# Kernel tuning notes

Measured on AMD Instinct MI355X. Metric: run time of the kernel, lower is better.

The kernel has to match this reference:

```python
import jax, jax.numpy as jnp
import numpy as np

B, S, D_MODEL = 2, 2048, 512
KEY_DIM, VALUE_DIM, OUTPUT_DIM, NUM_HEADS = 256, 256, 512, 8


def setup_inputs() -> dict:
    key = jax.random.key(0)
    ks = jax.random.split(key, 12)
    s = 0.02
    return {
        "V": jax.random.normal(ks[0], (B, S, D_MODEL), jnp.float32),
        "Q": jax.random.normal(ks[1], (B, S, D_MODEL), jnp.float32),
        "K": jax.random.normal(ks[2], (B, S, D_MODEL), jnp.float32),
        "mask": jax.random.normal(ks[3], (B, 1, S, S), jnp.float32),
        "Wq": jax.random.normal(ks[4], (D_MODEL, KEY_DIM), jnp.float32) * s,
        "bq": jnp.zeros((KEY_DIM,), jnp.float32),
        "Wk": jax.random.normal(ks[5], (D_MODEL, KEY_DIM), jnp.float32) * s,
        "bk": jnp.zeros((KEY_DIM,), jnp.float32),
        "Wv": jax.random.normal(ks[6], (D_MODEL, VALUE_DIM), jnp.float32) * s,
        "bv": jnp.zeros((VALUE_DIM,), jnp.float32),
        "Wo": jax.random.normal(ks[7], (VALUE_DIM, OUTPUT_DIM), jnp.float32) * s,
        "bo": jnp.zeros((OUTPUT_DIM,), jnp.float32),
    }


def _split_heads(x, num_heads):
    # [B, S, H*d] -> [B, H, S, d]
    b, s, hd = x.shape
    return x.reshape(b, s, num_heads, hd // num_heads).transpose(0, 2, 1, 3)


def reference(V, Q, K, mask, Wq, bq, Wk, bk, Wv, bv, Wo, bo):
    denom = jnp.sqrt(jnp.float32(KEY_DIM))  # NOTE: full key_dim, as in source
    q = _split_heads(Q @ Wq + bq, NUM_HEADS)  # [B,H,S,dk]
    k = _split_heads(K @ Wk + bk, NUM_HEADS)
    scores = jnp.einsum("bhqd,bhkd->bhqk", q, k) / denom
    scores = scores + mask  # soft (additive) mask
    weights = jax.nn.softmax(scores, axis=-1)
    v = _split_heads(V @ Wv + bv, NUM_HEADS)  # [B,H,S,dv]
    ctx = jnp.einsum("bhqk,bhkd->bhqd", weights, v)  # [B,H,S,dv]
    b, h, s, d = ctx.shape
    ctx = ctx.transpose(0, 2, 1, 3).reshape(b, s, h * d)  # merge heads
    return ctx @ Wo + bo
```

## Files before the change

### kernel.cpp

```cpp
#include <hip/hip_runtime.h>

typedef __attribute__((ext_vector_type(8))) short bf16x8;
typedef __attribute__((ext_vector_type(4))) float f32x4;

#define B_  2
#define S_  2048
#define DM  512
#define KD  256
#define HD  32
#define NH  8

__device__ __forceinline__ float bf2f(ushort u) {
    return __uint_as_float(((uint)u) << 16);
}
__device__ __forceinline__ ushort f2bf(float f) {
    uint x = __float_as_uint(f);
    return (ushort)((x + 0x7fffu + ((x >> 16) & 1u)) >> 16);
}
#define MFMA __builtin_amdgcn_mfma_f32_16x16x32_bf16

__device__ __forceinline__ int detect_isbf(const ushort* __restrict__ q)
{
    int lane = threadIdx.x & 63;
    int e = (q[lane] >> 7) & 0xFF;
    unsigned long long m = __ballot(e >= 100 && e <= 133);
    return __popcll(m) >= 58;
}

__global__ __launch_bounds__(256) void transpose_w(
    const void* __restrict__ Wq, const void* __restrict__ Wk, const void* __restrict__ Wv,
    const void* __restrict__ Wo,
    const void* __restrict__ bq, const void* __restrict__ bk,
    const void* __restrict__ bv, const void* __restrict__ bo,
    const ushort* __restrict__ qsrc,
    ushort* __restrict__ Wt, ushort* __restrict__ Wot, float* __restrict__ biasf)
{
    int isbf = detect_isbf(qsrc);
    int bid = blockIdx.x;
    if (bid >= 512) {
        for (int i = threadIdx.x; i < 1280; i += 256) {
            const void* bp; int off;
            if (i < 256)      { bp = bq; off = i; }
            else if (i < 512) { bp = bk; off = i - 256; }
            else if (i < 768) { bp = bv; off = i - 512; }
            else              { bp = bo; off = i - 768; }
            biasf[i] = isbf ? bf2f(((const ushort*)bp)[off]) : ((const float*)bp)[off];
        }
        return;
    }
    const void* W; int R, C; ushort* T;
    int m = bid >> 7, tix = bid & 127;
    if (m < 3) { W = (m == 0) ? Wq : (m == 1) ? Wk : Wv; R = 512; C = 256; T = Wt + m * 131072; }
    else       { W = Wo; R = 256; C = 512; T = Wot; }
    int tilesPerRow = C >> 5;
    int r0 = (tix / tilesPerRow) * 32, c0 = (tix % tilesPerRow) * 32;
    __shared__ float lds[32][33];
    int t = threadIdx.x;
    int rr = t >> 3, cc = (t & 7) * 4;
    if (isbf) {
        const ushort* Ws = (const ushort*)W;
        #pragma unroll
        for (int j = 0; j < 4; ++j) lds[rr][cc + j] = bf2f(Ws[(size_t)(r0 + rr) * C + c0 + cc + j]);
    } else {
        float4 v = *(const float4*)((const float*)W + (size_t)(r0 + rr) * C + c0 + cc);
        lds[rr][cc + 0] = v.x; lds[rr][cc + 1] = v.y; lds[rr][cc + 2] = v.z; lds[rr][cc + 3] = v.w;
    }
    __syncthreads();
    ushort4 o;
    o.x = f2bf(lds[cc + 0][rr]); o.y = f2bf(lds[cc + 1][rr]);
    o.z = f2bf(lds[cc + 2][rr]); o.w = f2bf(lds[cc + 3][rr]);
    *(ushort4*)(T + (size_t)(c0 + rr) * R + r0 + cc) = o;
}

__global__ __launch_bounds__(256) void qkv_gemm(
    const void* __restrict__ Q, const void* __restrict__ K, const void* __restrict__ V,
    const ushort* __restrict__ Wt, const float* __restrict__ biasf,
    ushort* __restrict__ qh, ushort* __restrict__ kh, ushort* __restrict__ vT)
{
    int isbf = detect_isbf((const ushort*)Q);
    int y = blockIdx.y;
    const void* X = (y == 0) ? Q : (y == 1) ? K : V;
    int wave = threadIdx.x >> 6, lane = threadIdx.x & 63;
    int l16 = lane & 15, quad = lane >> 4;
    int m0 = blockIdx.x * 32;
    int n0 = wave * 64;
    const ushort* W = Wt + (size_t)y * (256 * 512);

    auto loadA = [&](int ks, bf16x8* a) {
        #pragma unroll
        for (int i = 0; i < 2; ++i) {
            if (isbf) {
                a[i] = *(const bf16x8*)((const ushort*)X + (size_t)(m0 + 16 * i + l16) * 512 + ks + quad * 8);
            } else {
                const float* p = (const float*)X + (size_t)(m0 + 16 * i + l16) * 512 + ks + quad * 8;
                float4 f0 = *(const float4*)p, f1 = *(const float4*)(p + 4);
                bf16x8 v8;
                v8[0] = (short)f2bf(f0.x); v8[1] = (short)f2bf(f0.y);
                v8[2] = (short)f2bf(f0.z); v8[3] = (short)f2bf(f0.w);
                v8[4] = (short)f2bf(f1.x); v8[5] = (short)f2bf(f1.y);
                v8[6] = (short)f2bf(f1.z); v8[7] = (short)f2bf(f1.w);
                a[i] = v8;
            }
        }
    };
    auto loadB = [&](int ks, bf16x8* b) {
        #pragma unroll
        for (int j = 0; j < 4; ++j)
            b[j] = *(const bf16x8*)(W + (size_t)(n0 + 16 * j + l16) * 512 + ks + quad * 8);
    };

    f32x4 acc[2][4] = {};
    bf16x8 aC[2], bC[4], aN[2], bN[4];
    loadA(0, aC); loadB(0, bC);
    for (int ks = 0; ks < 512; ks += 32) {
        if (ks + 32 < 512) { loadA(ks + 32, aN); loadB(ks + 32, bN); }
        #pragma unroll
        for (int i = 0; i < 2; ++i)
            #pragma unroll
            for (int j = 0; j < 4; ++j)
                acc[i][j] = MFMA(aC[i], bC[j], acc[i][j], 0, 0, 0);
        aC[0] = aN[0]; aC[1] = aN[1];
        #pragma unroll
        for (int j = 0; j < 4; ++j) bC[j] = bN[j];
    }
    if (y < 2) {
        ushort* out = (y == 0) ? qh : kh;
        #pragma unroll
        for (int i = 0; i < 2; ++i) {
            #pragma unroll
            for (int j = 0; j < 4; ++j) {
                int n = n0 + 16 * j + l16;
                float bs = biasf[y * 256 + n];
                int h = n >> 5, d = n & 31;
                #pragma unroll
                for (int r = 0; r < 4; ++r) {
                    int rg = m0 + 16 * i + quad * 4 + r;
                    int bb = rg >> 11, ss = rg & 2047;
                    out[((((size_t)bb * NH + h) * S_ + ss) << 5) + d] = f2bf(acc[i][j][r] + bs);
                }
            }
        }
    } else {
        #pragma unroll
        for (int i = 0; i < 2; ++i) {
            int rg0 = m0 + 16 * i + quad * 4;
            int bb = rg0 >> 11, s0 = rg0 & 2047;
            #pragma unroll
            for (int j = 0; j < 4; ++j) {
                int n = n0 + 16 * j + l16;
                float bs = biasf[2 * 256 + n];
                int h = n >> 5, d = n & 31;
                ushort4 o;
                o.x = f2bf(acc[i][j][0] + bs); o.y = f2bf(acc[i][j][1] + bs);
                o.z = f2bf(acc[i][j][2] + bs); o.w = f2bf(acc[i][j][3] + bs);
                *(ushort4*)(vT + (((size_t)(bb * NH + h) * HD + d) * S_) + s0) = o;
            }
        }
    }
}

__global__ __launch_bounds__(256) void attn(
    const ushort* __restrict__ qh, const ushort* __restrict__ kh,
    const ushort* __restrict__ vT, const void* __restrict__ maskp,
    float* __restrict__ pO, float* __restrict__ pl)
{
    __shared__ __align__(16) ushort ldsP[4][16][72];
    int isbf;
    {
        int lane = threadIdx.x & 63;
        ushort u = ((const ushort*)maskp)[lane];
        int e = (u >> 7) & 0xFF;
        unsigned long long m = __ballot(e >= 100 && e <= 133);
        isbf = __popcll(m) >= 58;
    }
    int wave = threadIdx.x >> 6, lane = threadIdx.x & 63;
    int l16 = lane & 15, quad = lane >> 4;
    int wid = blockIdx.x * 4 + wave;
    int chunk = wid & 1, qt = (wid >> 1) & 127, bh = wid >> 8;
    int b = bh >> 3;
    int q0 = qt * 16;
    const ushort* qb = qh + (size_t)bh * S_ * HD;
    const ushort* kb = kh + (size_t)bh * S_ * HD;
    const ushort* vb = vT + (size_t)bh * HD * S_;
    const ushort* mbb = (const ushort*)maskp + (size_t)b * S_ * S_;
    const float*  mbf = (const float*)maskp  + (size_t)b * S_ * S_;
    size_t mbase = (size_t)(q0 + quad * 4) * S_ + l16;

    bf16x8 aq = *(const bf16x8*)(qb + (size_t)(q0 + l16) * HD + quad * 8);
    f32x4 O0 = {0, 0, 0, 0}, O1 = {0, 0, 0, 0};
    const f32x4 zero = {0, 0, 0, 0};
    float lsum[4] = {0, 0, 0, 0};

    auto loadT = [&](int k0, float* M, bf16x8* Kf, bf16x8* Vf) {
        if (isbf) {
            #pragma unroll
            for (int r = 0; r < 4; ++r) {
                const ushort* p = mbb + mbase + (size_t)r * S_ + k0;
                #pragma unroll
                for (int c = 0; c < 4; ++c) M[c * 4 + r] = bf2f(p[c * 16]);
            }
        } else {
            #pragma unroll
            for (int r = 0; r < 4; ++r) {
                const float* p = mbf + mbase + (size_t)r * S_ + k0;
                #pragma unroll
                for (int c = 0; c < 4; ++c) M[c * 4 + r] = p[c * 16];
            }
        }
        #pragma unroll
        for (int c = 0; c < 4; ++c)
            Kf[c] = *(const bf16x8*)(kb + (size_t)(k0 + c * 16 + l16) * HD + quad * 8);
        Vf[0] = *(const bf16x8*)(vb + (size_t)l16 * S_ + k0 + quad * 8);
        Vf[1] = *(const bf16x8*)(vb + (size_t)l16 * S_ + k0 + 32 + quad * 8);
        Vf[2] = *(const bf16x8*)(vb + (size_t)(16 + l16) * S_ + k0 + quad * 8);
        Vf[3] = *(const bf16x8*)(vb + (size_t)(16 + l16) * S_ + k0 + 32 + quad * 8);
    };

    auto tilestep = [&](float* M, bf16x8* Kf, bf16x8* Vf,
                        int nextk0, float* Mn, bf16x8* Kn, bf16x8* Vn) {
        if (nextk0 >= 0) loadT(nextk0, Mn, Kn, Vn);
        f32x4 Sc[4];
        #pragma unroll
        for (int c = 0; c < 4; ++c) Sc[c] = MFMA(aq, Kf[c], zero, 0, 0, 0);
        #pragma unroll
        for (int c = 0; c < 4; ++c) {
            #pragma unroll
            for (int r = 0; r < 4; ++r) {
                float s = fminf(fmaf(Sc[c][r], 0.0625f, M[c * 4 + r]), 30.0f);
                float p = __expf(s);
                lsum[r] += p;
                ldsP[wave][quad * 4 + r][c * 16 + l16] = f2bf(p);
            }
        }
        asm volatile("s_waitcnt lgkmcnt(0)" ::: "memory");
        bf16x8 aP0 = *(const bf16x8*)&ldsP[wave][l16][quad * 8];
        bf16x8 aP1 = *(const bf16x8*)&ldsP[wave][l16][32 + quad * 8];
        O0 = MFMA(aP0, Vf[0], O0, 0, 0, 0);
        O0 = MFMA(aP1, Vf[1], O0, 0, 0, 0);
        O1 = MFMA(aP0, Vf[2], O1, 0, 0, 0);
        O1 = MFMA(aP1, Vf[3], O1, 0, 0, 0);
    };

    int kbase = chunk * 1024;
    float Ma[16], Mb2[16]; bf16x8 Ka[4], Kb2[4], Va[4], Vb2[4];
    loadT(kbase, Ma, Ka, Va);
    for (int t = 0; t < 16; t += 2) {
        tilestep(Ma, Ka, Va, kbase + (t + 1) * 64, Mb2, Kb2, Vb2);
        tilestep(Mb2, Kb2, Vb2, (t + 2 < 16) ? kbase + (t + 2) * 64 : -1, Ma, Ka, Va);
    }

    float* po = pO + (size_t)wid * 512;
    #pragma unroll
    for (int r = 0; r < 4; ++r) {
        int row = quad * 4 + r;
        po[row * 32 + l16]      = O0[r];
        po[row * 32 + 16 + l16] = O1[r];
        float sthis = lsum[r];
        #pragma unroll
        for (int off = 8; off; off >>= 1) sthis += __shfl_xor(sthis, off, 16);
        if (l16 == 0) pl[wid * 16 + row] = sthis;
    }
}

__global__ __launch_bounds__(256) void out_proj(
    const float* __restrict__ pO, const float* __restrict__ pl,
    const ushort* __restrict__ Wot, const float* __restrict__ biasf,
    float* __restrict__ out)
{
    int wave = threadIdx.x >> 6, lane = threadIdx.x & 63;
    int l16 = lane & 15, quad = lane >> 4;
    int m0 = (blockIdx.x >> 1) * 32;
    int n0 = (blockIdx.x & 1) * 256 + wave * 64;
    f32x4 acc[2][4] = {};
    for (int ks = 0; ks < 256; ks += 32) {
        int h = ks >> 5;
        bf16x8 a[2], b[4];
        #pragma unroll
        for (int i = 0; i < 2; ++i) {
            int row = m0 + 16 * i + l16;
            int bb = row >> 11, s = row & 2047;
            int qt = s >> 4, r16 = s & 15;
            int wid0 = ((bb * NH + h) << 8) | (qt << 1);
            const float* p0 = pO + (size_t)wid0 * 512 + r16 * 32 + quad * 8;
            float4 x0 = *(const float4*)p0,         x1 = *(const float4*)(p0 + 4);
            float4 y0 = *(const float4*)(p0 + 512), y1 = *(const float4*)(p0 + 516);
            float il = 1.0f / (pl[wid0 * 16 + r16] + pl[(wid0 + 1) * 16 + r16]);
            bf16x8 v8;
            v8[0] = (short)f2bf((x0.x + y0.x) * il); v8[1] = (short)f2bf((x0.y + y0.y) * il);
            v8[2] = (short)f2bf((x0.z + y0.z) * il); v8[3] = (short)f2bf((x0.w + y0.w) * il);
            v8[4] = (short)f2bf((x1.x + y1.x) * il); v8[5] = (short)f2bf((x1.y + y1.y) * il);
            v8[6] = (short)f2bf((x1.z + y1.z) * il); v8[7] = (short)f2bf((x1.w + y1.w) * il);
            a[i] = v8;
        }
        #pragma unroll
        for (int j = 0; j < 4; ++j)
            b[j] = *(const bf16x8*)(Wot + (size_t)(n0 + 16 * j + l16) * 256 + ks + quad * 8);
        #pragma unroll
        for (int i = 0; i < 2; ++i)
            #pragma unroll
            for (int j = 0; j < 4; ++j)
                acc[i][j] = MFMA(a[i], b[j], acc[i][j], 0, 0, 0);
    }
    #pragma unroll
    for (int i = 0; i < 2; ++i) {
        #pragma unroll
        for (int j = 0; j < 4; ++j) {
            int n = n0 + 16 * j + l16;
            float bs = biasf[768 + n];
            #pragma unroll
            for (int r = 0; r < 4; ++r) {
                int rg = m0 + 16 * i + quad * 4 + r;
                out[(size_t)rg * DM + n] = acc[i][j][r] + bs;
            }
        }
    }
}

extern "C" void kernel_launch(void* const* d_in, const int* in_sizes, int n_in,
                              void* d_out, int out_size, void* d_ws, size_t ws_size,
                              hipStream_t stream)
{
    const void* V    = d_in[0];
    const void* Q    = d_in[1];
    const void* K    = d_in[2];
    const void* mask = d_in[3];
    const void* Wq = d_in[4];  const void* bq = d_in[5];
    const void* Wk = d_in[6];  const void* bk = d_in[7];
    const void* Wv = d_in[8];  const void* bv = d_in[9];
    const void* Wo = d_in[10]; const void* bo = d_in[11];
    float* out = (float*)d_out;

    char* ws = (char*)d_ws;
    float*  biasf = (float*)ws;
    ushort* Wt  = (ushort*)(ws + 8192);
    ushort* Wot = Wt  + 393216;
    ushort* qh  = Wot + 131072;
    ushort* kh  = qh  + 1048576;
    ushort* vT  = kh  + 1048576;
    float*  pO  = (float*)(vT + 1048576);
    float*  pl  = pO + 4096 * 512;

    transpose_w<<<513, 256, 0, stream>>>(Wq, Wk, Wv, Wo, bq, bk, bv, bo,
                                         (const ushort*)Q, Wt, Wot, biasf);
    qkv_gemm<<<dim3(128, 3), 256, 0, stream>>>(Q, K, V, Wt, biasf, qh, kh, vT);
    attn<<<1024, 256, 0, stream>>>(qh, kh, vT, mask, pO, pl);
    out_proj<<<256, 256, 0, stream>>>(pO, pl, Wot, biasf, out);
}
```

Baseline: 208.5 us.

## Split attention keys into more chunks and halve GEMM row tiles for occupancy

The attention kernel now splits each query tile's key range into 2^chsh chunks instead of a fixed 2, choosing 4 chunks when the workspace is large enough. That doubles the attention grid, and out_proj sums the extra partial outputs and denominators. The QKV and output projection GEMMs use 16-row tiles instead of 32, doubling their block counts so the GPU has more blocks to schedule. In exchange there is more partial-result traffic and reduction work in out_proj, and less reuse of the weight tiles per block.

Result: slower. 228.7 us (+9.7%).

```diff
diff --git a/kernel.cpp b/kernel.cpp
--- a/kernel.cpp
+++ b/kernel.cpp
@@ -82,25 +82,22 @@
     const void* X = (y == 0) ? Q : (y == 1) ? K : V;
     int wave = threadIdx.x >> 6, lane = threadIdx.x & 63;
     int l16 = lane & 15, quad = lane >> 4;
-    int m0 = blockIdx.x * 32;
+    int m0 = blockIdx.x * 16;
     int n0 = wave * 64;
     const ushort* W = Wt + (size_t)y * (256 * 512);
 
     auto loadA = [&](int ks, bf16x8* a) {
-        #pragma unroll
-        for (int i = 0; i < 2; ++i) {
-            if (isbf) {
-                a[i] = *(const bf16x8*)((const ushort*)X + (size_t)(m0 + 16 * i + l16) * 512 + ks + quad * 8);
-            } else {
-                const float* p = (const float*)X + (size_t)(m0 + 16 * i + l16) * 512 + ks + quad * 8;
-                float4 f0 = *(const float4*)p, f1 = *(const float4*)(p + 4);
-                bf16x8 v8;
-                v8[0] = (short)f2bf(f0.x); v8[1] = (short)f2bf(f0.y);
-                v8[2] = (short)f2bf(f0.z); v8[3] = (short)f2bf(f0.w);
-                v8[4] = (short)f2bf(f1.x); v8[5] = (short)f2bf(f1.y);
-                v8[6] = (short)f2bf(f1.z); v8[7] = (short)f2bf(f1.w);
-                a[i] = v8;
-            }
+        if (isbf) {
+            *a = *(const bf16x8*)((const ushort*)X + (size_t)(m0 + l16) * 512 + ks + quad * 8);
+        } else {
+            const float* p = (const float*)X + (size_t)(m0 + l16) * 512 + ks + quad * 8;
+            float4 f0 = *(const float4*)p, f1 = *(const float4*)(p + 4);
+            bf16x8 v8;
+            v8[0] = (short)f2bf(f0.x); v8[1] = (short)f2bf(f0.y);
+            v8[2] = (short)f2bf(f0.z); v8[3] = (short)f2bf(f0.w);
+            v8[4] = (short)f2bf(f1.x); v8[5] = (short)f2bf(f1.y);
+            v8[6] = (short)f2bf(f1.z); v8[7] = (short)f2bf(f1.w);
+            *a = v8;
         }
     };
     auto loadB = [&](int ks, bf16x8* b) {
@@ -109,52 +106,44 @@
             b[j] = *(const bf16x8*)(W + (size_t)(n0 + 16 * j + l16) * 512 + ks + quad * 8);
     };
 
-    f32x4 acc[2][4] = {};
-    bf16x8 aC[2], bC[4], aN[2], bN[4];
-    loadA(0, aC); loadB(0, bC);
+    f32x4 acc[4] = {};
+    bf16x8 aC, bC[4], aN, bN[4];
+    loadA(0, &aC); loadB(0, bC);
     for (int ks = 0; ks < 512; ks += 32) {
-        if (ks + 32 < 512) { loadA(ks + 32, aN); loadB(ks + 32, bN); }
-        #pragma unroll
-        for (int i = 0; i < 2; ++i)
-            #pragma unroll
-            for (int j = 0; j < 4; ++j)
-                acc[i][j] = MFMA(aC[i], bC[j], acc[i][j], 0, 0, 0);
-        aC[0] = aN[0]; aC[1] = aN[1];
+        if (ks + 32 < 512) { loadA(ks + 32, &aN); loadB(ks + 32, bN); }
+        #pragma unroll
+        for (int j = 0; j < 4; ++j)
+            acc[j] = MFMA(aC, bC[j], acc[j], 0, 0, 0);
+        aC = aN;
         #pragma unroll
         for (int j = 0; j < 4; ++j) bC[j] = bN[j];
     }
     if (y < 2) {
         ushort* out = (y == 0) ? qh : kh;
         #pragma unroll
-        for (int i = 0; i < 2; ++i) {
+        for (int j = 0; j < 4; ++j) {
+            int n = n0 + 16 * j + l16;
+            float bs = biasf[y * 256 + n];
+            int h = n >> 5, d = n & 31;
             #pragma unroll
-            for (int j = 0; j < 4; ++j) {
-                int n = n0 + 16 * j + l16;
-                float bs = biasf[y * 256 + n];
-                int h = n >> 5, d = n & 31;
-                #pragma unroll
-                for (int r = 0; r < 4; ++r) {
-                    int rg = m0 + 16 * i + quad * 4 + r;
-                    int bb = rg >> 11, ss = rg & 2047;
-                    out[((((size_t)bb * NH + h) * S_ + ss) << 5) + d] = f2bf(acc[i][j][r] + bs);
-                }
+            for (int r = 0; r < 4; ++r) {
+                int rg = m0 + quad * 4 + r;
+                int bb = rg >> 11, ss = rg & 2047;
+                out[((((size_t)bb * NH + h) * S_ + ss) << 5) + d] = f2bf(acc[j][r] + bs);
             }
         }
     } else {
-        #pragma unroll
-        for (int i = 0; i < 2; ++i) {
-            int rg0 = m0 + 16 * i + quad * 4;
-            int bb = rg0 >> 11, s0 = rg0 & 2047;
-            #pragma unroll
-            for (int j = 0; j < 4; ++j) {
-                int n = n0 + 16 * j + l16;
-                float bs = biasf[2 * 256 + n];
-                int h = n >> 5, d = n & 31;
-                ushort4 o;
-                o.x = f2bf(acc[i][j][0] + bs); o.y = f2bf(acc[i][j][1] + bs);
-                o.z = f2bf(acc[i][j][2] + bs); o.w = f2bf(acc[i][j][3] + bs);
-                *(ushort4*)(vT + (((size_t)(bb * NH + h) * HD + d) * S_) + s0) = o;
-            }
+        int rg0 = m0 + quad * 4;
+        int bb = rg0 >> 11, s0 = rg0 & 2047;
+        #pragma unroll
+        for (int j = 0; j < 4; ++j) {
+            int n = n0 + 16 * j + l16;
+            float bs = biasf[2 * 256 + n];
+            int h = n >> 5, d = n & 31;
+            ushort4 o;
+            o.x = f2bf(acc[j][0] + bs); o.y = f2bf(acc[j][1] + bs);
+            o.z = f2bf(acc[j][2] + bs); o.w = f2bf(acc[j][3] + bs);
+            *(ushort4*)(vT + (((size_t)(bb * NH + h) * HD + d) * S_) + s0) = o;
         }
     }
 }
@@ -162,7 +151,7 @@
 __global__ __launch_bounds__(256) void attn(
     const ushort* __restrict__ qh, const ushort* __restrict__ kh,
     const ushort* __restrict__ vT, const void* __restrict__ maskp,
-    float* __restrict__ pO, float* __restrict__ pl)
+    float* __restrict__ pO, float* __restrict__ pl, int chsh)
 {
     __shared__ __align__(16) ushort ldsP[4][16][72];
     int isbf;
@@ -176,7 +165,9 @@
     int wave = threadIdx.x >> 6, lane = threadIdx.x & 63;
     int l16 = lane & 15, quad = lane >> 4;
     int wid = blockIdx.x * 4 + wave;
-    int chunk = wid & 1, qt = (wid >> 1) & 127, bh = wid >> 8;
+    int chunk = wid & ((1 << chsh) - 1);
+    int qt = (wid >> chsh) & 127;
+    int bh = wid >> (chsh + 7);
     int b = bh >> 3;
     int q0 = qt * 16;
     const ushort* qb = qh + (size_t)bh * S_ * HD;
@@ -241,12 +232,13 @@
         O1 = MFMA(aP1, Vf[3], O1, 0, 0, 0);
     };
 
-    int kbase = chunk * 1024;
+    int kbase = chunk << (11 - chsh);
+    int NT = 16 >> (chsh - 1);
     float Ma[16], Mb2[16]; bf16x8 Ka[4], Kb2[4], Va[4], Vb2[4];
     loadT(kbase, Ma, Ka, Va);
-    for (int t = 0; t < 16; t += 2) {
+    for (int t = 0; t < NT; t += 2) {
         tilestep(Ma, Ka, Va, kbase + (t + 1) * 64, Mb2, Kb2, Vb2);
-        tilestep(Mb2, Kb2, Vb2, (t + 2 < 16) ? kbase + (t + 2) * 64 : -1, Ma, Ka, Va);
+        tilestep(Mb2, Kb2, Vb2, (t + 2 < NT) ? kbase + (t + 2) * 64 : -1, Ma, Ka, Va);
     }
 
     float* po = pO + (size_t)wid * 512;
@@ -265,53 +257,54 @@
 __global__ __launch_bounds__(256) void out_proj(
     const float* __restrict__ pO, const float* __restrict__ pl,
     const ushort* __restrict__ Wot, const float* __restrict__ biasf,
-    float* __restrict__ out)
+    float* __restrict__ out, int chsh)
 {
     int wave = threadIdx.x >> 6, lane = threadIdx.x & 63;
     int l16 = lane & 15, quad = lane >> 4;
-    int m0 = (blockIdx.x >> 1) * 32;
+    int m0 = (blockIdx.x >> 1) * 16;
     int n0 = (blockIdx.x & 1) * 256 + wave * 64;
-    f32x4 acc[2][4] = {};
+    int CH = 1 << chsh;
+    f32x4 acc[4] = {};
     for (int ks = 0; ks < 256; ks += 32) {
         int h = ks >> 5;
-        bf16x8 a[2], b[4];
-        #pragma unroll
-        for (int i = 0; i < 2; ++i) {
-            int row = m0 + 16 * i + l16;
+        bf16x8 a, b[4];
+        {
+            int row = m0 + l16;
             int bb = row >> 11, s = row & 2047;
             int qt = s >> 4, r16 = s & 15;
-            int wid0 = ((bb * NH + h) << 8) | (qt << 1);
-            const float* p0 = pO + (size_t)wid0 * 512 + r16 * 32 + quad * 8;
-            float4 x0 = *(const float4*)p0,         x1 = *(const float4*)(p0 + 4);
-            float4 y0 = *(const float4*)(p0 + 512), y1 = *(const float4*)(p0 + 516);
-            float il = 1.0f / (pl[wid0 * 16 + r16] + pl[(wid0 + 1) * 16 + r16]);
+            int wid0 = ((bb * NH + h) * 128 + qt) << chsh;
+            float s8[8] = {0, 0, 0, 0, 0, 0, 0, 0};
+            float lacc = 0.0f;
+            for (int cc = 0; cc < CH; ++cc) {
+                const float* p = pO + ((size_t)(wid0 + cc) << 9) + r16 * 32 + quad * 8;
+                float4 u0 = *(const float4*)p, u1 = *(const float4*)(p + 4);
+                s8[0] += u0.x; s8[1] += u0.y; s8[2] += u0.z; s8[3] += u0.w;
+                s8[4] += u1.x; s8[5] += u1.y; s8[6] += u1.z; s8[7] += u1.w;
+                lacc += pl[(wid0 + cc) * 16 + r16];
+            }
+            float il = 1.0f / lacc;
             bf16x8 v8;
-            v8[0] = (short)f2bf((x0.x + y0.x) * il); v8[1] = (short)f2bf((x0.y + y0.y) * il);
-            v8[2] = (short)f2bf((x0.z + y0.z) * il); v8[3] = (short)f2bf((x0.w + y0.w) * il);
-            v8[4] = (short)f2bf((x1.x + y1.x) * il); v8[5] = (short)f2bf((x1.y + y1.y) * il);
-            v8[6] = (short)f2bf((x1.z + y1.z) * il); v8[7] = (short)f2bf((x1.w + y1.w) * il);
-            a[i] = v8;
+            v8[0] = (short)f2bf(s8[0] * il); v8[1] = (short)f2bf(s8[1] * il);
+            v8[2] = (short)f2bf(s8[2] * il); v8[3] = (short)f2bf(s8[3] * il);
+            v8[4] = (short)f2bf(s8[4] * il); v8[5] = (short)f2bf(s8[5] * il);
+            v8[6] = (short)f2bf(s8[6] * il); v8[7] = (short)f2bf(s8[7] * il);
+            a = v8;
         }
         #pragma unroll
         for (int j = 0; j < 4; ++j)
             b[j] = *(const bf16x8*)(Wot + (size_t)(n0 + 16 * j + l16) * 256 + ks + quad * 8);
         #pragma unroll
-        for (int i = 0; i < 2; ++i)
-            #pragma unroll
-            for (int j = 0; j < 4; ++j)
-                acc[i][j] = MFMA(a[i], b[j], acc[i][j], 0, 0, 0);
+        for (int j = 0; j < 4; ++j)
+            acc[j] = MFMA(a, b[j], acc[j], 0, 0, 0);
     }
     #pragma unroll
-    for (int i = 0; i < 2; ++i) {
-        #pragma unroll
-        for (int j = 0; j < 4; ++j) {
-            int n = n0 + 16 * j + l16;
-            float bs = biasf[768 + n];
-            #pragma unroll
-            for (int r = 0; r < 4; ++r) {
-                int rg = m0 + 16 * i + quad * 4 + r;
-                out[(size_t)rg * DM + n] = acc[i][j][r] + bs;
-            }
+    for (int j = 0; j < 4; ++j) {
+        int n = n0 + 16 * j + l16;
+        float bs = biasf[768 + n];
+        #pragma unroll
+        for (int r = 0; r < 4; ++r) {
+            int rg = m0 + quad * 4 + r;
+            out[(size_t)rg * DM + n] = acc[j][r] + bs;
         }
     }
 }
@@ -338,11 +331,12 @@
     ushort* kh  = qh  + 1048576;
     ushort* vT  = kh  + 1048576;
     float*  pO  = (float*)(vT + 1048576);
-    float*  pl  = pO + 4096 * 512;
+    int chsh = (ws_size >= 24649728u) ? 2 : 1;
+    float*  pl  = pO + ((size_t)2048 << chsh) * 512;
 
     transpose_w<<<513, 256, 0, stream>>>(Wq, Wk, Wv, Wo, bq, bk, bv, bo,
                                          (const ushort*)Q, Wt, Wot, biasf);
-    qkv_gemm<<<dim3(128, 3), 256, 0, stream>>>(Q, K, V, Wt, biasf, qh, kh, vT);
-    attn<<<1024, 256, 0, stream>>>(qh, kh, vT, mask, pO, pl);
-    out_proj<<<256, 256, 0, stream>>>(pO, pl, Wot, biasf, out);
-}
+    qkv_gemm<<<dim3(256, 3), 256, 0, stream>>>(Q, K, V, Wt, biasf, qh, kh, vT);
+    attn<<<512 << chsh, 256, 0, stream>>>(qh, kh, vT, mask, pO, pl, chsh);
+    out_proj<<<512, 256, 0, stream>>>(pO, pl, Wot, biasf, out, chsh);
+}
```

## Process two query tiles per wave in attention and pre-tile weight layouts

Applied to the files above, without the earlier changes.

Each attention wave now handles 32 query rows instead of 16, so every K and V fragment load is shared by two query tiles, and the grid is halved. The loads are split into separate K, mask and V prefetches placed at different points in the step to overlap them with compute. Transposed weights are stored in an MFMA-fragment-tiled layout so the B-operand loads in the QKV and output GEMMs read contiguous memory. The cost is more registers per wave (two sets of mask values and accumulators), which may lower occupancy, and only 512 workgroups for attention.

New measurement: 189.5 us. 9.1% less time.

```diff
diff --git a/kernel.cpp b/kernel.cpp
--- a/kernel.cpp
+++ b/kernel.cpp
@@ -69,7 +69,8 @@
     ushort4 o;
     o.x = f2bf(lds[cc + 0][rr]); o.y = f2bf(lds[cc + 1][rr]);
     o.z = f2bf(lds[cc + 2][rr]); o.w = f2bf(lds[cc + 3][rr]);
-    *(ushort4*)(T + (size_t)(c0 + rr) * R + r0 + cc) = o;
+    int n = c0 + rr, k = r0 + cc;
+    *(ushort4*)(T + ((((size_t)(n >> 4) * (R >> 3) + (k >> 3)) * 16 + (n & 15)) << 3) + (k & 7)) = o;
 }
 
 __global__ __launch_bounds__(256) void qkv_gemm(
@@ -106,7 +107,7 @@
     auto loadB = [&](int ks, bf16x8* b) {
         #pragma unroll
         for (int j = 0; j < 4; ++j)
-            b[j] = *(const bf16x8*)(W + (size_t)(n0 + 16 * j + l16) * 512 + ks + quad * 8);
+            b[j] = *(const bf16x8*)(W + (((size_t)((n0 >> 4) + j) * 64 + (ks >> 3) + quad) * 16 + l16) * 8);
     };
 
     f32x4 acc[2][4] = {};
@@ -164,7 +165,7 @@
     const ushort* __restrict__ vT, const void* __restrict__ maskp,
     float* __restrict__ pO, float* __restrict__ pl)
 {
-    __shared__ __align__(16) ushort ldsP[4][16][72];
+    __shared__ __align__(16) ushort ldsP[4][2][16][72];
     int isbf;
     {
         int lane = threadIdx.x & 63;
@@ -176,9 +177,9 @@
     int wave = threadIdx.x >> 6, lane = threadIdx.x & 63;
     int l16 = lane & 15, quad = lane >> 4;
     int wid = blockIdx.x * 4 + wave;
-    int chunk = wid & 1, qt = (wid >> 1) & 127, bh = wid >> 8;
+    int chunk = wid & 1, qt32 = (wid >> 1) & 63, bh = wid >> 7;
     int b = bh >> 3;
-    int q0 = qt * 16;
+    int q0 = qt32 * 32;
     const ushort* qb = qh + (size_t)bh * S_ * HD;
     const ushort* kb = kh + (size_t)bh * S_ * HD;
     const ushort* vb = vT + (size_t)bh * HD * S_;
@@ -186,79 +187,111 @@
     const float*  mbf = (const float*)maskp  + (size_t)b * S_ * S_;
     size_t mbase = (size_t)(q0 + quad * 4) * S_ + l16;
 
-    bf16x8 aq = *(const bf16x8*)(qb + (size_t)(q0 + l16) * HD + quad * 8);
-    f32x4 O0 = {0, 0, 0, 0}, O1 = {0, 0, 0, 0};
+    bf16x8 aq0 = *(const bf16x8*)(qb + (size_t)(q0 + l16) * HD + quad * 8);
+    bf16x8 aq1 = *(const bf16x8*)(qb + (size_t)(q0 + 16 + l16) * HD + quad * 8);
+    f32x4 O00 = {0,0,0,0}, O01 = {0,0,0,0}, O10 = {0,0,0,0}, O11 = {0,0,0,0};
     const f32x4 zero = {0, 0, 0, 0};
-    float lsum[4] = {0, 0, 0, 0};
-
-    auto loadT = [&](int k0, float* M, bf16x8* Kf, bf16x8* Vf) {
+    float lsum0[4] = {0,0,0,0}, lsum1[4] = {0,0,0,0};
+    float M0[16], M1[16];
+    bf16x8 Vf[4];
+
+    auto loadK = [&](int k0, bf16x8* Kf) {
+        #pragma unroll
+        for (int c = 0; c < 4; ++c)
+            Kf[c] = *(const bf16x8*)(kb + (size_t)(k0 + c * 16 + l16) * HD + quad * 8);
+    };
+    auto loadM = [&](int k0) {
         if (isbf) {
             #pragma unroll
             for (int r = 0; r < 4; ++r) {
                 const ushort* p = mbb + mbase + (size_t)r * S_ + k0;
                 #pragma unroll
-                for (int c = 0; c < 4; ++c) M[c * 4 + r] = bf2f(p[c * 16]);
+                for (int c = 0; c < 4; ++c) M0[c * 4 + r] = bf2f(p[c * 16]);
+                p += (size_t)16 * S_;
+                #pragma unroll
+                for (int c = 0; c < 4; ++c) M1[c * 4 + r] = bf2f(p[c * 16]);
             }
         } else {
             #pragma unroll
             for (int r = 0; r < 4; ++r) {
                 const float* p = mbf + mbase + (size_t)r * S_ + k0;
                 #pragma unroll
-                for (int c = 0; c < 4; ++c) M[c * 4 + r] = p[c * 16];
-            }
-        }
-        #pragma unroll
-        for (int c = 0; c < 4; ++c)
-            Kf[c] = *(const bf16x8*)(kb + (size_t)(k0 + c * 16 + l16) * HD + quad * 8);
+                for (int c = 0; c < 4; ++c) M0[c * 4 + r] = p[c * 16];
+                p += (size_t)16 * S_;
+                #pragma unroll
+                for (int c = 0; c < 4; ++c) M1[c * 4 + r] = p[c * 16];
+            }
+        }
+    };
+    auto loadV = [&](int k0) {
         Vf[0] = *(const bf16x8*)(vb + (size_t)l16 * S_ + k0 + quad * 8);
         Vf[1] = *(const bf16x8*)(vb + (size_t)l16 * S_ + k0 + 32 + quad * 8);
         Vf[2] = *(const bf16x8*)(vb + (size_t)(16 + l16) * S_ + k0 + quad * 8);
         Vf[3] = *(const bf16x8*)(vb + (size_t)(16 + l16) * S_ + k0 + 32 + quad * 8);
     };
 
-    auto tilestep = [&](float* M, bf16x8* Kf, bf16x8* Vf,
-                        int nextk0, float* Mn, bf16x8* Kn, bf16x8* Vn) {
-        if (nextk0 >= 0) loadT(nextk0, Mn, Kn, Vn);
-        f32x4 Sc[4];
-        #pragma unroll
-        for (int c = 0; c < 4; ++c) Sc[c] = MFMA(aq, Kf[c], zero, 0, 0, 0);
+    auto substep = [&](bf16x8* Kcur, int nextk0, bf16x8* Knext) {
+        if (nextk0 >= 0) loadK(nextk0, Knext);
+        f32x4 Sc0[4], Sc1[4];
+        #pragma unroll
+        for (int c = 0; c < 4; ++c) Sc0[c] = MFMA(aq0, Kcur[c], zero, 0, 0, 0);
+        #pragma unroll
+        for (int c = 0; c < 4; ++c) Sc1[c] = MFMA(aq1, Kcur[c], zero, 0, 0, 0);
         #pragma unroll
         for (int c = 0; c < 4; ++c) {
             #pragma unroll
             for (int r = 0; r < 4; ++r) {
-                float s = fminf(fmaf(Sc[c][r], 0.0625f, M[c * 4 + r]), 30.0f);
+                float s = fminf(fmaf(Sc0[c][r], 0.0625f, M0[c * 4 + r]), 30.0f);
                 float p = __expf(s);
-                lsum[r] += p;
-                ldsP[wave][quad * 4 + r][c * 16 + l16] = f2bf(p);
-            }
-        }
+                lsum0[r] += p;
+                ldsP[wave][0][quad * 4 + r][c * 16 + l16] = f2bf(p);
+                float s1 = fminf(fmaf(Sc1[c][r], 0.0625f, M1[c * 4 + r]), 30.0f);
+                float p1 = __expf(s1);
+                lsum1[r] += p1;
+                ldsP[wave][1][quad * 4 + r][c * 16 + l16] = f2bf(p1);
+            }
+        }
+        if (nextk0 >= 0) loadM(nextk0);
         asm volatile("s_waitcnt lgkmcnt(0)" ::: "memory");
-        bf16x8 aP0 = *(const bf16x8*)&ldsP[wave][l16][quad * 8];
-        bf16x8 aP1 = *(const bf16x8*)&ldsP[wave][l16][32 + quad * 8];
-        O0 = MFMA(aP0, Vf[0], O0, 0, 0, 0);
-        O0 = MFMA(aP1, Vf[1], O0, 0, 0, 0);
-        O1 = MFMA(aP0, Vf[2], O1, 0, 0, 0);
-        O1 = MFMA(aP1, Vf[3], O1, 0, 0, 0);
+        bf16x8 aP00 = *(const bf16x8*)&ldsP[wave][0][l16][quad * 8];
+        bf16x8 aP01 = *(const bf16x8*)&ldsP[wave][0][l16][32 + quad * 8];
+        bf16x8 aP10 = *(const bf16x8*)&ldsP[wave][1][l16][quad * 8];
+        bf16x8 aP11 = *(const bf16x8*)&ldsP[wave][1][l16][32 + quad * 8];
+        O00 = MFMA(aP00, Vf[0], O00, 0, 0, 0);
+        O00 = MFMA(aP01, Vf[1], O00, 0, 0, 0);
+        O01 = MFMA(aP00, Vf[2], O01, 0, 0, 0);
+        O01 = MFMA(aP01, Vf[3], O01, 0, 0, 0);
+        O10 = MFMA(aP10, Vf[0], O10, 0, 0, 0);
+        O10 = MFMA(aP11, Vf[1], O10, 0, 0, 0);
+        O11 = MFMA(aP10, Vf[2], O11, 0, 0, 0);
+        O11 = MFMA(aP11, Vf[3], O11, 0, 0, 0);
+        if (nextk0 >= 0) loadV(nextk0);
     };
 
     int kbase = chunk * 1024;
-    float Ma[16], Mb2[16]; bf16x8 Ka[4], Kb2[4], Va[4], Vb2[4];
-    loadT(kbase, Ma, Ka, Va);
+    bf16x8 Ka[4], Kb2[4];
+    loadK(kbase, Ka); loadM(kbase); loadV(kbase);
     for (int t = 0; t < 16; t += 2) {
-        tilestep(Ma, Ka, Va, kbase + (t + 1) * 64, Mb2, Kb2, Vb2);
-        tilestep(Mb2, Kb2, Vb2, (t + 2 < 16) ? kbase + (t + 2) * 64 : -1, Ma, Ka, Va);
-    }
-
-    float* po = pO + (size_t)wid * 512;
+        substep(Ka, kbase + (t + 1) * 64, Kb2);
+        substep(Kb2, (t + 2 < 16) ? kbase + (t + 2) * 64 : -1, Ka);
+    }
+
     #pragma unroll
-    for (int r = 0; r < 4; ++r) {
-        int row = quad * 4 + r;
-        po[row * 32 + l16]      = O0[r];
-        po[row * 32 + 16 + l16] = O1[r];
-        float sthis = lsum[r];
-        #pragma unroll
-        for (int off = 8; off; off >>= 1) sthis += __shfl_xor(sthis, off, 16);
-        if (l16 == 0) pl[wid * 16 + row] = sthis;
+    for (int tile = 0; tile < 2; ++tile) {
+        int wid16 = ((bh * 128) + (qt32 * 2 + tile)) * 2 + chunk;
+        float* po = pO + (size_t)wid16 * 512;
+        f32x4 Oa = tile ? O10 : O00, Ob = tile ? O11 : O01;
+        float* ls = tile ? lsum1 : lsum0;
+        #pragma unroll
+        for (int r = 0; r < 4; ++r) {
+            int row = quad * 4 + r;
+            po[row * 32 + l16]      = Oa[r];
+            po[row * 32 + 16 + l16] = Ob[r];
+            float sthis = ls[r];
+            #pragma unroll
+            for (int off = 8; off; off >>= 1) sthis += __shfl_xor(sthis, off, 16);
+            if (l16 == 0) pl[wid16 * 16 + row] = sthis;
+        }
     }
 }
 
@@ -294,7 +327,7 @@
         }
         #pragma unroll
         for (int j = 0; j < 4; ++j)
-            b[j] = *(const bf16x8*)(Wot + (size_t)(n0 + 16 * j + l16) * 256 + ks + quad * 8);
+            b[j] = *(const bf16x8*)(Wot + (((size_t)((n0 >> 4) + j) * 32 + (ks >> 3) + quad) * 16 + l16) * 8);
         #pragma unroll
         for (int i = 0; i < 2; ++i)
             #pragma unroll
@@ -343,6 +376,6 @@
     transpose_w<<<513, 256, 0, stream>>>(Wq, Wk, Wv, Wo, bq, bk, bv, bo,
                                          (const ushort*)Q, Wt, Wot, biasf);
     qkv_gemm<<<dim3(128, 3), 256, 0, stream>>>(Q, K, V, Wt, biasf, qh, kh, vT);
-    attn<<<1024, 256, 0, stream>>>(qh, kh, vT, mask, pO, pl);
+    attn<<<512, 256, 0, stream>>>(qh, kh, vT, mask, pO, pl);
     out_proj<<<256, 256, 0, stream>>>(pO, pl, Wot, biasf, out);
 }
```
